# Optimization experiments

Hardware: AMD Instinct MI355X
Metric: run time of the kernel (lower is better)

The kernel has to match this reference:

```python
import jax, jax.numpy as jnp
import numpy as np
import math

N, T, D_MODEL = 4, 2048, 1024
NHEAD = 16
HEAD_DIM = D_MODEL // NHEAD
ROTARY_DIM = 64
WINDOW = (128, 128)
ROPE_BASE = 10000.0


def _rope_cos_sin(seq_len, rotary_dim, dtype):
    # non-interleaved (GPT-NeoX style) rotary embedding tables
    inv_freq = 1.0 / (ROPE_BASE ** (jnp.arange(0, rotary_dim, 2, dtype=jnp.float32) / rotary_dim))
    t = jnp.arange(seq_len, dtype=jnp.float32)
    freqs = jnp.outer(t, inv_freq)  # [T, rotary_dim//2]
    return jnp.cos(freqs).astype(dtype), jnp.sin(freqs).astype(dtype)


def _apply_rope(x, cos, sin):
    # x: [N, T, H, D]; rotate first ROTARY_DIM dims, pass the rest through
    r = ROTARY_DIM
    x_rot, x_pass = x[..., :r], x[..., r:]
    x1, x2 = x_rot[..., : r // 2], x_rot[..., r // 2 :]
    c = cos[None, :, None, :]
    s = sin[None, :, None, :]
    out = jnp.concatenate([x1 * c - x2 * s, x1 * s + x2 * c], axis=-1)
    return jnp.concatenate([out, x_pass], axis=-1)


def _sliding_window_bias(seq_len, window, dtype):
    i = jnp.arange(seq_len)[:, None]
    j = jnp.arange(seq_len)[None, :]
    # triu(diag=-w0) & tril(diag=w1): keep j - i in [-w0, w1]
    keep = (j - i >= -window[0]) & (j - i <= window[1])
    return jnp.where(keep, jnp.zeros((), dtype), jnp.full((), -jnp.inf, dtype))


def setup_inputs() -> dict:
    key = jax.random.key(0)
    k1, k2, k3 = jax.random.split(key, 3)
    x = jax.random.normal(k1, (N, T, D_MODEL), dtype=jnp.float32)
    Wqkv = jax.random.normal(k2, (D_MODEL, 3 * D_MODEL), dtype=jnp.float32) * (1.0 / math.sqrt(D_MODEL))
    Wout = jax.random.normal(k3, (D_MODEL, D_MODEL), dtype=jnp.float32) * (1.0 / math.sqrt(D_MODEL))
    bout = jnp.zeros((D_MODEL,), dtype=jnp.float32)
    return {"x": x, "Wqkv": Wqkv, "Wout": Wout, "bout": bout}


def reference(x, Wqkv, Wout, bout):
    n, t, _ = x.shape
    qkv = (x @ Wqkv).reshape(n, t, 3, NHEAD, HEAD_DIM)
    q, k, v = qkv[:, :, 0], qkv[:, :, 1], qkv[:, :, 2]  # each [N, T, H, D]
    cos, sin = _rope_cos_sin(t, ROTARY_DIM, x.dtype)
    q = _apply_rope(q, cos, sin)
    k = _apply_rope(k, cos, sin)
    scale = 1.0 / math.sqrt(HEAD_DIM)
    bias = _sliding_window_bias(t, WINDOW, x.dtype)  # [T, T]
    scores = jnp.einsum("bthd,bshd->bhts", q, k) * scale + bias[None, None]
    attn = jax.nn.softmax(scores, axis=-1)
    out = jnp.einsum("bhts,bshd->bthd", attn, v).reshape(n, t, D_MODEL)
    return out @ Wout + bout
```

## Files before the change

kernel.cpp:

```cpp
#include <hip/hip_runtime.h>
#include <hip/hip_bf16.h>
#include <cstdint>
#include <cstddef>

typedef __bf16 bf16_t;
typedef bf16_t bf16x8 __attribute__((ext_vector_type(8)));
typedef float f32x4 __attribute__((ext_vector_type(4)));
typedef unsigned short ushort_t;

#define T_SEQ 2048
#define DM 1024
#define NH 16
#define HD 64
#define WIN 128
#define ROPE_C 0.28782313662425572f
#define SCALE_LOG2E 0.18033688011112042f
#define ATT_M 16.0f

__device__ __forceinline__ ushort_t f2bf(float f) {
    union { float f; unsigned u; } v; v.f = f;
    unsigned r = v.u + 0x7fff + ((v.u >> 16) & 1);
    return (ushort_t)(r >> 16);
}
__device__ __forceinline__ float sane(float v, float sent) {
    return (fabsf(v) < 1e30f) ? v : sent;
}
__device__ __forceinline__ void gld16(const ushort_t* g, ushort_t* l) {
    __builtin_amdgcn_global_load_lds(
        (const __attribute__((address_space(1))) unsigned int*)g,
        (__attribute__((address_space(3))) unsigned int*)l, 16, 0, 0);
}

__global__ __launch_bounds__(256) void kzero_f(float* __restrict__ p) {
    size_t i = ((size_t)blockIdx.x * 256 + threadIdx.x) * 4;
    float4 z; z.x = z.y = z.z = z.w = 0.f;
    *(float4*)(p + i) = z;
}

__device__ __forceinline__ void trans_f2b_tile(const float* __restrict__ in,
                                               ushort_t* __restrict__ out,
                                               int R, int C, int c0, int r0) {
    __shared__ __align__(16) ushort_t tile[64][72];
    const int tid = threadIdx.x;
    const int rl = tid >> 2, q4 = tid & 3;
    const float* src = in + (size_t)(r0 + rl) * C + c0 + q4 * 16;
    ushort_t cv[16];
#pragma unroll
    for (int i = 0; i < 4; i++) {
        float4 f = *(const float4*)(src + i * 4);
        cv[i * 4 + 0] = f2bf(f.x); cv[i * 4 + 1] = f2bf(f.y);
        cv[i * 4 + 2] = f2bf(f.z); cv[i * 4 + 3] = f2bf(f.w);
    }
    *(uint4*)&tile[rl][q4 * 16]     = *(uint4*)&cv[0];
    *(uint4*)&tile[rl][q4 * 16 + 8] = *(uint4*)&cv[8];
    __syncthreads();
    const int cl = tid >> 2;
    ushort_t tmp[16];
#pragma unroll
    for (int i = 0; i < 16; i++) tmp[i] = tile[q4 * 16 + i][cl];
    ushort_t* dst = out + (size_t)(c0 + cl) * R + r0 + q4 * 16;
    *(uint4*)(dst)     = *(uint4*)&tmp[0];
    *(uint4*)(dst + 8) = *(uint4*)&tmp[8];
}

__global__ __launch_bounds__(256) void prep(const float* __restrict__ x,
                                            const float* __restrict__ Wqkv,
                                            const float* __restrict__ Wout,
                                            ushort_t* __restrict__ xb,
                                            ushort_t* __restrict__ WqkvT,
                                            ushort_t* __restrict__ WoutT) {
    const int bx = blockIdx.x;
    if (bx < 4096) {
        size_t i = ((size_t)bx * 256 + threadIdx.x) * 8;
        float4 a0 = *(const float4*)(x + i);
        float4 a1 = *(const float4*)(x + i + 4);
        ushort_t cv[8];
        cv[0] = f2bf(a0.x); cv[1] = f2bf(a0.y); cv[2] = f2bf(a0.z); cv[3] = f2bf(a0.w);
        cv[4] = f2bf(a1.x); cv[5] = f2bf(a1.y); cv[6] = f2bf(a1.z); cv[7] = f2bf(a1.w);
        *(uint4*)(xb + i) = *(uint4*)cv;
    } else if (bx < 4864) {
        int tb = bx - 4096;
        trans_f2b_tile(Wqkv, WqkvT, 1024, 3072, (tb % 48) * 64, (tb / 48) * 64);
    } else {
        int tb = bx - 4864;
        trans_f2b_tile(Wout, WoutT, 1024, 1024, (tb & 15) * 64, (tb >> 4) * 64);
    }
}

#define BM 128
#define BN 256
#define BK 64
#define KTILES 16
#define LBUF ((BM + BN) * BK)
#define LTOT (3 * LBUF)

__device__ __forceinline__ void gemm_core(const ushort_t* __restrict__ Agl,
                                          const ushort_t* __restrict__ Bgl,
                                          ushort_t* L, int m0, int n0,
                                          f32x4 (&acc)[4][4]) {
    const int tid = threadIdx.x;
    const int lane = tid & 63, w = tid >> 6;
    const int wr = w >> 2, wc = w & 3;
    const int c = lane & 15, g = lane >> 4;
    const int rr = tid >> 3;
    const int cc8 = ((tid & 7) ^ (rr & 7)) * 8;
    const int lw = (w * 8) * BK;
    const int arow = wr * 64 + c;
    const int brow = wc * 64 + c;
    const int cxk0 = ((0 + g) ^ (c & 7)) * 8;
    const int cxk1 = ((4 + g) ^ (c & 7)) * 8;

#pragma unroll
    for (int mi = 0; mi < 4; ++mi)
#pragma unroll
        for (int ni = 0; ni < 4; ++ni)
#pragma unroll
            for (int r = 0; r < 4; ++r) acc[mi][ni][r] = 0.f;

    auto STAGE = [&](int kt, int bo) {
        const int k0 = kt * BK;
        const ushort_t* ga = Agl + (size_t)(m0 + rr) * 1024 + k0 + cc8;
        ushort_t* la = L + bo + lw;
        gld16(ga, la);
        gld16(ga + 64 * 1024, la + 64 * BK);
        const ushort_t* gb = Bgl + (size_t)(n0 + rr) * 1024 + k0 + cc8;
        ushort_t* lb = la + BM * BK;
#pragma unroll
        for (int s = 0; s < 4; ++s)
            gld16(gb + (size_t)(s * 64) * 1024, lb + s * 64 * BK);
    };

    STAGE(0, 0);
    STAGE(1, LBUF);
    asm volatile("s_waitcnt vmcnt(6)\n\ts_barrier" ::: "memory");

    int bcur = 0;
    for (int kt = 0; kt < KTILES; ++kt) {
        int bst = bcur + 2 * LBUF; if (bst >= LTOT) bst -= LTOT;
        if (kt + 2 < KTILES) STAGE(kt + 2, bst);

        const ushort_t* Lb = L + bcur;
        const ushort_t* Bb = Lb + BM * BK;
        bf16x8 af[4][2], bfr[4][2];
#pragma unroll
        for (int mi = 0; mi < 4; ++mi) {
            const ushort_t* p = Lb + (arow + mi * 16) * BK;
            af[mi][0] = *(const bf16x8*)(p + cxk0);
            af[mi][1] = *(const bf16x8*)(p + cxk1);
        }
#pragma unroll
        for (int ni = 0; ni < 4; ++ni) {
            const ushort_t* p = Bb + (brow + ni * 16) * BK;
            bfr[ni][0] = *(const bf16x8*)(p + cxk0);
            bfr[ni][1] = *(const bf16x8*)(p + cxk1);
        }
        __builtin_amdgcn_s_setprio(1);
#pragma unroll
        for (int mi = 0; mi < 4; ++mi)
#pragma unroll
            for (int ni = 0; ni < 4; ++ni) {
                acc[mi][ni] = __builtin_amdgcn_mfma_f32_16x16x32_bf16(
                    af[mi][0], bfr[ni][0], acc[mi][ni], 0, 0, 0);
                acc[mi][ni] = __builtin_amdgcn_mfma_f32_16x16x32_bf16(
                    af[mi][1], bfr[ni][1], acc[mi][ni], 0, 0, 0);
            }
        __builtin_amdgcn_s_setprio(0);
        if (kt < KTILES - 2)
            asm volatile("s_waitcnt vmcnt(6)\n\ts_barrier" ::: "memory");
        else if (kt == KTILES - 2)
            asm volatile("s_waitcnt vmcnt(0)\n\ts_barrier" ::: "memory");
        bcur += LBUF; if (bcur == LTOT) bcur = 0;
    }
}

__global__ __launch_bounds__(512) void gemm_qkv(const ushort_t* __restrict__ A,
                                                const ushort_t* __restrict__ Bt,
                                                ushort_t* __restrict__ Qr,
                                                ushort_t* __restrict__ Kr,
                                                ushort_t* __restrict__ Vt) {
    __shared__ __align__(16) ushort_t L[LTOT];
    const int m0 = blockIdx.x * BM, n0 = blockIdx.y * BN;
    f32x4 acc[4][4];
    gemm_core(A, Bt, L, m0, n0, acc);

    const int lane = threadIdx.x & 63, w = threadIdx.x >> 6;
    const int wr = w >> 2, wc = w & 3;
    const int c = lane & 15, g = lane >> 4;
    const int nb = n0 + wc * 64;
    const int sec = nb >> 10;
    const int h = (nb >> 6) & 15;
    const int mrow = m0 + wr * 64;

    if (sec < 2) {
        ushort_t* dst = (sec == 0) ? Qr : Kr;
        const float invf0 = __expf(-(float)(c) * ROPE_C);
        const float invf1 = __expf(-(float)(16 + c) * ROPE_C);
#pragma unroll
        for (int mi = 0; mi < 4; ++mi)
#pragma unroll
            for (int r = 0; r < 4; ++r) {
                int tg = mrow + mi * 16 + g * 4 + r;
                int nB = tg >> 11, t = tg & (T_SEQ - 1);
                float a0 = (float)t * invf0, a1 = (float)t * invf1;
                float s0 = __sinf(a0), c0 = __cosf(a0);
                float s1 = __sinf(a1), c1 = __cosf(a1);
                size_t base = ((size_t)(nB * NH + h) * T_SEQ + t) * 64;
                float x1a = acc[mi][0][r], x2a = acc[mi][2][r];
                float x1b = acc[mi][1][r], x2b = acc[mi][3][r];
                dst[base + c]      = f2bf(sane(x1a * c0 - x2a * s0, 1e3f));
                dst[base + 16 + c] = f2bf(sane(x1b * c1 - x2b * s1, 1e3f));
                dst[base + 32 + c] = f2bf(sane(x1a * s0 + x2a * c0, 1e3f));
                dst[base + 48 + c] = f2bf(sane(x1b * s1 + x2b * c1, 1e3f));
            }
    } else {
#pragma unroll
        for (int mi = 0; mi < 4; ++mi) {
            int tgb = mrow + mi * 16 + g * 4;
            int nB = tgb >> 11, t = tgb & (T_SEQ - 1);
            size_t vrow = (size_t)(nB * NH + h) * 64 * T_SEQ;
#pragma unroll
            for (int ni = 0; ni < 4; ++ni) {
                ushort4 pk;
                pk.x = f2bf(sane(acc[mi][ni][0], 1e3f));
                pk.y = f2bf(sane(acc[mi][ni][1], 1e3f));
                pk.z = f2bf(sane(acc[mi][ni][2], 1e3f));
                pk.w = f2bf(sane(acc[mi][ni][3], 1e3f));
                *(ushort4*)&Vt[vrow + (size_t)(ni * 16 + c) * T_SEQ + t] = pk;
            }
        }
    }
}

__global__ __launch_bounds__(512) void gemm_out(const ushort_t* __restrict__ A,
                                                const ushort_t* __restrict__ Bt,
                                                float* __restrict__ C,
                                                const float* __restrict__ bias) {
    __shared__ __align__(16) ushort_t L[LTOT];
    const int m0 = blockIdx.x * BM, n0 = blockIdx.y * BN;
    f32x4 acc[4][4];
    gemm_core(A, Bt, L, m0, n0, acc);

    const int lane = threadIdx.x & 63, w = threadIdx.x >> 6;
    const int wr = w >> 2, wc = w & 3;
    const int c = lane & 15, g = lane >> 4;
#pragma unroll
    for (int ni = 0; ni < 4; ++ni) {
        int col = n0 + wc * 64 + ni * 16 + c;
        float bv = bias[col];
#pragma unroll
        for (int mi = 0; mi < 4; ++mi)
#pragma unroll
            for (int r = 0; r < 4; ++r) {
                int rowi = m0 + wr * 64 + mi * 16 + g * 4 + r;
                C[(size_t)rowi * 1024 + col] = sane(acc[mi][ni][r] + bv, 1e8f);
            }
    }
}

__global__ __launch_bounds__(256) void attn_swin(const ushort_t* __restrict__ Qr,
                                                 const ushort_t* __restrict__ Kr,
                                                 const ushort_t* __restrict__ Vt,
                                                 ushort_t* __restrict__ O) {
    __shared__ __align__(16) ushort_t Ks[32 * 72];
    __shared__ __align__(16) ushort_t Vs[64 * 72];
    __shared__ __align__(16) ushort_t pbuf[4][2][16 * 32];
    const int tid = threadIdx.x;
    const int wid = tid >> 6, lane = tid & 63;
    const int qb = (blockIdx.x & 15) * 128;
    const int h = (blockIdx.x >> 4) & 15, n = blockIdx.x >> 8;
    const int c = lane & 15, g = lane >> 4;
    const size_t hb = ((size_t)(n * NH + h)) * T_SEQ * 64;
    const int t0s[2] = { qb + wid * 16, qb + 64 + wid * 16 };
    const int ks_row = tid >> 3, ks_col = (tid & 7) * 8;
    const int vs_row = tid >> 2, vs_col = (tid & 3) * 8;

    bf16x8 qf0[2], qf1[2];
#pragma unroll
    for (int sub = 0; sub < 2; sub++) {
        qf0[sub] = *(const bf16x8*)(Qr + hb + (size_t)(t0s[sub] + c) * 64 + g * 8);
        qf1[sub] = *(const bf16x8*)(Qr + hb + (size_t)(t0s[sub] + c) * 64 + 32 + g * 8);
    }

    f32x4 o[2][4];
    float l_r[2][4];
#pragma unroll
    for (int sub = 0; sub < 2; sub++)
#pragma unroll
        for (int i = 0; i < 4; i++) {
            l_r[sub][i] = 0.f;
#pragma unroll
            for (int r = 0; r < 4; r++) o[sub][i][r] = 0.f;
        }

    int sB_lo = qb - WIN;        if (sB_lo < 0) sB_lo = 0;
    int sB_hi = qb + 127 + WIN;  if (sB_hi > T_SEQ - 1) sB_hi = T_SEQ - 1;

    uint4 kreg = *(const uint4*)(Kr + hb + (size_t)(sB_lo + ks_row) * 64 + ks_col);
    uint4 vreg = *(const uint4*)(Vt + hb + (size_t)vs_row * T_SEQ + sB_lo + vs_col);

    for (int s0 = sB_lo; s0 <= sB_hi; s0 += 32) {
        __syncthreads();
        *(uint4*)&Ks[ks_row * 72 + ks_col] = kreg;
        *(uint4*)&Vs[vs_row * 72 + vs_col] = vreg;
        __syncthreads();
        int s1 = s0 + 32;
        if (s1 <= sB_hi) {
            kreg = *(const uint4*)(Kr + hb + (size_t)(s1 + ks_row) * 64 + ks_col);
            vreg = *(const uint4*)(Vt + hb + (size_t)vs_row * T_SEQ + s1 + vs_col);
        }
        bool act[2];
#pragma unroll
        for (int sub = 0; sub < 2; sub++)
            act[sub] = !(s0 > t0s[sub] + 143 || s0 + 31 < t0s[sub] - WIN);
        if (!act[0] && !act[1]) continue;

#pragma unroll
        for (int sub = 0; sub < 2; sub++) {
            if (!act[sub]) continue;
            const int t0 = t0s[sub];
            f32x4 S[2];
#pragma unroll
            for (int sh = 0; sh < 2; sh++) {
                bf16x8 kf0 = *(const bf16x8*)&Ks[(sh * 16 + c) * 72 + g * 8];
                bf16x8 kf1 = *(const bf16x8*)&Ks[(sh * 16 + c) * 72 + 32 + g * 8];
                f32x4 z;
#pragma unroll
                for (int r = 0; r < 4; r++) z[r] = 0.f;
                z = __builtin_amdgcn_mfma_f32_16x16x32_bf16(qf0[sub], kf0, z, 0, 0, 0);
                z = __builtin_amdgcn_mfma_f32_16x16x32_bf16(qf1[sub], kf1, z, 0, 0, 0);
                S[sh] = z;
            }
            const bool interior = (s0 >= t0 - 113) && (s0 <= t0 + 97);
            ushort_t* pb = pbuf[wid][sub];
            if (interior) {
#pragma unroll
                for (int sh = 0; sh < 2; sh++)
#pragma unroll
                    for (int r = 0; r < 4; r++) {
                        float p = exp2f(S[sh][r] * SCALE_LOG2E - ATT_M);
                        l_r[sub][r] += p;
                        pb[(g * 4 + r) * 32 + sh * 16 + c] = f2bf(p);
                    }
            } else {
#pragma unroll
                for (int sh = 0; sh < 2; sh++)
#pragma unroll
                    for (int r = 0; r < 4; r++) {
                        int s = s0 + sh * 16 + c;
                        int q = t0 + g * 4 + r;
                        bool keep = (s - q >= -WIN) && (s - q <= WIN);
                        float v = keep ? S[sh][r] * SCALE_LOG2E : -1e30f;
                        float p = exp2f(v - ATT_M);
                        l_r[sub][r] += p;
                        pb[(g * 4 + r) * 32 + sh * 16 + c] = f2bf(p);
                    }
            }
        }
        __asm__ volatile("s_waitcnt lgkmcnt(0)" ::: "memory");
#pragma unroll
        for (int sub = 0; sub < 2; sub++) {
            if (!act[sub]) continue;
            bf16x8 pf = *(const bf16x8*)&pbuf[wid][sub][c * 32 + g * 8];
#pragma unroll
            for (int di = 0; di < 4; di++) {
                bf16x8 vf = *(const bf16x8*)&Vs[(di * 16 + c) * 72 + g * 8];
                o[sub][di] = __builtin_amdgcn_mfma_f32_16x16x32_bf16(pf, vf, o[sub][di], 0, 0, 0);
            }
        }
        __asm__ volatile("" ::: "memory");
    }

#pragma unroll
    for (int sub = 0; sub < 2; sub++) {
#pragma unroll
        for (int off = 1; off < 16; off <<= 1)
#pragma unroll
            for (int r = 0; r < 4; r++)
                l_r[sub][r] += __shfl_xor(l_r[sub][r], off, 64);
        float inv[4];
#pragma unroll
        for (int r = 0; r < 4; r++) inv[r] = __builtin_amdgcn_rcpf(l_r[sub][r]);
#pragma unroll
        for (int di = 0; di < 4; di++)
#pragma unroll
            for (int r = 0; r < 4; r++) {
                int q = t0s[sub] + g * 4 + r;
                float val = o[sub][di][r] * inv[r];
                O[((size_t)(n * T_SEQ + q)) * DM + h * 64 + di * 16 + c] =
                    f2bf(sane(val, 1e6f));
            }
    }
}

extern "C" void kernel_launch(void* const* d_in, const int* in_sizes, int n_in,
                              void* d_out, int out_size, void* d_ws, size_t ws_size,
                              hipStream_t stream) {
    const float* x    = (const float*)d_in[0];
    const float* Wqkv = (const float*)d_in[1];
    const float* Wout = (const float*)d_in[2];
    const float* bout = (const float*)d_in[3];
    float* out = (float*)d_out;

    const size_t NEED = 72ull << 20;
    if (ws_size < NEED) {
        kzero_f<<<dim3(8192), 256, 0, stream>>>(out);
        return;
    }
    char* ws = (char*)d_ws;
    ushort_t* WqkvT = (ushort_t*)(ws);
    ushort_t* WoutT = (ushort_t*)(ws + (6ull << 20));
    ushort_t* Qr    = (ushort_t*)(ws + (8ull << 20));
    ushort_t* Kr    = (ushort_t*)(ws + (24ull << 20));
    ushort_t* Vt    = (ushort_t*)(ws + (40ull << 20));
    ushort_t* xb    = (ushort_t*)(ws + (56ull << 20));
    ushort_t* Oat   = xb;

    prep<<<dim3(5120), 256, 0, stream>>>(x, Wqkv, Wout, xb, WqkvT, WoutT);
    gemm_qkv<<<dim3(64, 12), 512, 0, stream>>>(xb, WqkvT, Qr, Kr, Vt);
    attn_swin<<<dim3(1024), 256, 0, stream>>>(Qr, Kr, Vt, Oat);
    gemm_out<<<dim3(64, 4), 512, 0, stream>>>(Oat, WoutT, out, bout);
}
```

Measured before the change: 210.2 us.

## Restructure GEMM core to 4 waves with 128x64 per-wave tiles and BK=32

```diff
diff --git a/kernel.cpp b/kernel.cpp
--- a/kernel.cpp
+++ b/kernel.cpp
@@ -89,29 +89,25 @@
 
 #define BM 128
 #define BN 256
-#define BK 64
-#define KTILES 16
+#define BK 32
+#define KTILES 32
 #define LBUF ((BM + BN) * BK)
 #define LTOT (3 * LBUF)
 
 __device__ __forceinline__ void gemm_core(const ushort_t* __restrict__ Agl,
                                           const ushort_t* __restrict__ Bgl,
                                           ushort_t* L, int m0, int n0,
-                                          f32x4 (&acc)[4][4]) {
+                                          f32x4 (&acc)[8][4]) {
     const int tid = threadIdx.x;
     const int lane = tid & 63, w = tid >> 6;
-    const int wr = w >> 2, wc = w & 3;
     const int c = lane & 15, g = lane >> 4;
-    const int rr = tid >> 3;
-    const int cc8 = ((tid & 7) ^ (rr & 7)) * 8;
-    const int lw = (w * 8) * BK;
-    const int arow = wr * 64 + c;
-    const int brow = wc * 64 + c;
-    const int cxk0 = ((0 + g) ^ (c & 7)) * 8;
-    const int cxk1 = ((4 + g) ^ (c & 7)) * 8;
-
-#pragma unroll
-    for (int mi = 0; mi < 4; ++mi)
+    const int sv   = (lane & 7) ^ (lane >> 3);
+    const int grow = 2 * (lane >> 3) + (sv >> 2);
+    const int gcol = (sv & 3) * 8;
+    const int loff = (c >> 1) * 64 + (((((c & 1) << 2) | g) ^ ((c >> 1) & 7)) * 8);
+
+#pragma unroll
+    for (int mi = 0; mi < 8; ++mi)
 #pragma unroll
         for (int ni = 0; ni < 4; ++ni)
 #pragma unroll
@@ -119,15 +115,16 @@
 
     auto STAGE = [&](int kt, int bo) {
         const int k0 = kt * BK;
-        const ushort_t* ga = Agl + (size_t)(m0 + rr) * 1024 + k0 + cc8;
-        ushort_t* la = L + bo + lw;
-        gld16(ga, la);
-        gld16(ga + 64 * 1024, la + 64 * BK);
-        const ushort_t* gb = Bgl + (size_t)(n0 + rr) * 1024 + k0 + cc8;
-        ushort_t* lb = la + BM * BK;
-#pragma unroll
-        for (int s = 0; s < 4; ++s)
-            gld16(gb + (size_t)(s * 64) * 1024, lb + s * 64 * BK);
+#pragma unroll
+        for (int j = 0; j < 2; ++j) {
+            const ushort_t* ga = Agl + (size_t)(m0 + 32 * w + 16 * j + grow) * 1024 + k0 + gcol;
+            gld16(ga, &L[bo + (w * 2 + j) * 512]);
+        }
+#pragma unroll
+        for (int j = 0; j < 4; ++j) {
+            const ushort_t* gb = Bgl + (size_t)(n0 + 64 * w + 16 * j + grow) * 1024 + k0 + gcol;
+            gld16(gb, &L[bo + BM * BK + (w * 4 + j) * 512]);
+        }
     };
 
     STAGE(0, 0);
@@ -139,31 +136,33 @@
         int bst = bcur + 2 * LBUF; if (bst >= LTOT) bst -= LTOT;
         if (kt + 2 < KTILES) STAGE(kt + 2, bst);
 
-        const ushort_t* Lb = L + bcur;
-        const ushort_t* Bb = Lb + BM * BK;
-        bf16x8 af[4][2], bfr[4][2];
-#pragma unroll
-        for (int mi = 0; mi < 4; ++mi) {
-            const ushort_t* p = Lb + (arow + mi * 16) * BK;
-            af[mi][0] = *(const bf16x8*)(p + cxk0);
-            af[mi][1] = *(const bf16x8*)(p + cxk1);
-        }
-#pragma unroll
-        for (int ni = 0; ni < 4; ++ni) {
-            const ushort_t* p = Bb + (brow + ni * 16) * BK;
-            bfr[ni][0] = *(const bf16x8*)(p + cxk0);
-            bfr[ni][1] = *(const bf16x8*)(p + cxk1);
-        }
+        const ushort_t* La = L + bcur;
+        const ushort_t* Bb = La + BM * BK;
+        bf16x8 bfr[4], af0[4], af1[4];
+#pragma unroll
+        for (int ni = 0; ni < 4; ++ni)
+            bfr[ni] = *(const bf16x8*)&Bb[w * 2048 + ni * 512 + loff];
+#pragma unroll
+        for (int mi = 0; mi < 4; ++mi)
+            af0[mi] = *(const bf16x8*)&La[mi * 512 + loff];
         __builtin_amdgcn_s_setprio(1);
 #pragma unroll
         for (int mi = 0; mi < 4; ++mi)
 #pragma unroll
-            for (int ni = 0; ni < 4; ++ni) {
+            for (int ni = 0; ni < 4; ++ni)
                 acc[mi][ni] = __builtin_amdgcn_mfma_f32_16x16x32_bf16(
-                    af[mi][0], bfr[ni][0], acc[mi][ni], 0, 0, 0);
-                acc[mi][ni] = __builtin_amdgcn_mfma_f32_16x16x32_bf16(
-                    af[mi][1], bfr[ni][1], acc[mi][ni], 0, 0, 0);
-            }
+                    af0[mi], bfr[ni], acc[mi][ni], 0, 0, 0);
+        __builtin_amdgcn_s_setprio(0);
+#pragma unroll
+        for (int mi = 0; mi < 4; ++mi)
+            af1[mi] = *(const bf16x8*)&La[(mi + 4) * 512 + loff];
+        __builtin_amdgcn_s_setprio(1);
+#pragma unroll
+        for (int mi = 0; mi < 4; ++mi)
+#pragma unroll
+            for (int ni = 0; ni < 4; ++ni)
+                acc[mi + 4][ni] = __builtin_amdgcn_mfma_f32_16x16x32_bf16(
+                    af1[mi], bfr[ni], acc[mi + 4][ni], 0, 0, 0);
         __builtin_amdgcn_s_setprio(0);
         if (kt < KTILES - 2)
             asm volatile("s_waitcnt vmcnt(6)\n\ts_barrier" ::: "memory");
@@ -173,33 +172,31 @@
     }
 }
 
-__global__ __launch_bounds__(512) void gemm_qkv(const ushort_t* __restrict__ A,
-                                                const ushort_t* __restrict__ Bt,
-                                                ushort_t* __restrict__ Qr,
-                                                ushort_t* __restrict__ Kr,
-                                                ushort_t* __restrict__ Vt) {
+__global__ __launch_bounds__(256, 2) void gemm_qkv(const ushort_t* __restrict__ A,
+                                                   const ushort_t* __restrict__ Bt,
+                                                   ushort_t* __restrict__ Qr,
+                                                   ushort_t* __restrict__ Kr,
+                                                   ushort_t* __restrict__ Vt) {
     __shared__ __align__(16) ushort_t L[LTOT];
     const int m0 = blockIdx.x * BM, n0 = blockIdx.y * BN;
-    f32x4 acc[4][4];
+    f32x4 acc[8][4];
     gemm_core(A, Bt, L, m0, n0, acc);
 
     const int lane = threadIdx.x & 63, w = threadIdx.x >> 6;
-    const int wr = w >> 2, wc = w & 3;
     const int c = lane & 15, g = lane >> 4;
-    const int nb = n0 + wc * 64;
+    const int nb = n0 + w * 64;
     const int sec = nb >> 10;
     const int h = (nb >> 6) & 15;
-    const int mrow = m0 + wr * 64;
 
     if (sec < 2) {
         ushort_t* dst = (sec == 0) ? Qr : Kr;
         const float invf0 = __expf(-(float)(c) * ROPE_C);
         const float invf1 = __expf(-(float)(16 + c) * ROPE_C);
 #pragma unroll
-        for (int mi = 0; mi < 4; ++mi)
+        for (int mi = 0; mi < 8; ++mi)
 #pragma unroll
             for (int r = 0; r < 4; ++r) {
-                int tg = mrow + mi * 16 + g * 4 + r;
+                int tg = m0 + mi * 16 + g * 4 + r;
                 int nB = tg >> 11, t = tg & (T_SEQ - 1);
                 float a0 = (float)t * invf0, a1 = (float)t * invf1;
                 float s0 = __sinf(a0), c0 = __cosf(a0);
@@ -214,8 +211,8 @@
             }
     } else {
 #pragma unroll
-        for (int mi = 0; mi < 4; ++mi) {
-            int tgb = mrow + mi * 16 + g * 4;
+        for (int mi = 0; mi < 8; ++mi) {
+            int tgb = m0 + mi * 16 + g * 4;
             int nB = tgb >> 11, t = tgb & (T_SEQ - 1);
             size_t vrow = (size_t)(nB * NH + h) * 64 * T_SEQ;
 #pragma unroll
@@ -231,27 +228,26 @@
     }
 }
 
-__global__ __launch_bounds__(512) void gemm_out(const ushort_t* __restrict__ A,
-                                                const ushort_t* __restrict__ Bt,
-                                                float* __restrict__ C,
-                                                const float* __restrict__ bias) {
+__global__ __launch_bounds__(256, 2) void gemm_out(const ushort_t* __restrict__ A,
+                                                   const ushort_t* __restrict__ Bt,
+                                                   float* __restrict__ C,
+                                                   const float* __restrict__ bias) {
     __shared__ __align__(16) ushort_t L[LTOT];
     const int m0 = blockIdx.x * BM, n0 = blockIdx.y * BN;
-    f32x4 acc[4][4];
+    f32x4 acc[8][4];
     gemm_core(A, Bt, L, m0, n0, acc);
 
     const int lane = threadIdx.x & 63, w = threadIdx.x >> 6;
-    const int wr = w >> 2, wc = w & 3;
     const int c = lane & 15, g = lane >> 4;
 #pragma unroll
     for (int ni = 0; ni < 4; ++ni) {
-        int col = n0 + wc * 64 + ni * 16 + c;
+        int col = n0 + w * 64 + ni * 16 + c;
         float bv = bias[col];
 #pragma unroll
-        for (int mi = 0; mi < 4; ++mi)
+        for (int mi = 0; mi < 8; ++mi)
 #pragma unroll
             for (int r = 0; r < 4; ++r) {
-                int rowi = m0 + wr * 64 + mi * 16 + g * 4 + r;
+                int rowi = m0 + mi * 16 + g * 4 + r;
                 C[(size_t)rowi * 1024 + col] = sane(acc[mi][ni][r] + bv, 1e8f);
             }
     }
@@ -416,7 +412,7 @@
     ushort_t* Oat   = xb;
 
     prep<<<dim3(5120), 256, 0, stream>>>(x, Wqkv, Wout, xb, WqkvT, WoutT);
-    gemm_qkv<<<dim3(64, 12), 512, 0, stream>>>(xb, WqkvT, Qr, Kr, Vt);
+    gemm_qkv<<<dim3(64, 12), 256, 0, stream>>>(xb, WqkvT, Qr, Kr, Vt);
     attn_swin<<<dim3(1024), 256, 0, stream>>>(Qr, Kr, Vt, Oat);
-    gemm_out<<<dim3(64, 4), 512, 0, stream>>>(Oat, WoutT, out, bout);
-}
+    gemm_out<<<dim3(64, 4), 256, 0, stream>>>(Oat, WoutT, out, bout);
+}
```

Result: no change. 209.7 us (median of 3 runs) (-0.2%).
